# Optimization experiments

Measured on AMD Instinct MI355X. Metric: run time of the kernel, lower is better.

Reference implementation:

```python
import jax, jax.numpy as jnp
import numpy as np


def _relative_position_index(ws):
    # matches SpatialAttention.build with qWh=qWw=kWh=kWw=ws
    coords = np.stack(np.meshgrid(np.arange(ws), np.arange(ws), indexing='ij'))
    cf = coords.reshape(2, -1)  # [2, N]
    rel = (cf[:, :, None] - cf[:, None, :]).transpose(1, 2, 0)  # [N, N, 2]
    rel[:, :, 0] += ws - 1
    rel[:, :, 1] += ws - 1
    rel[:, :, 0] *= 2 * ws - 1
    return rel.sum(-1)  # [N, N] int in [0, (2*ws-1)^2)


def _shift_mask(H, W, ws, ss):
    # standard Swin shifted-window attention mask: [num_windows, N, N]
    img = np.zeros((H, W))
    cnt = 0
    for h in (slice(0, -ws), slice(-ws, -ss), slice(-ss, None)):
        for w in (slice(0, -ws), slice(-ws, -ss), slice(-ss, None)):
            img[h, w] = cnt
            cnt += 1
    win = img.reshape(H // ws, ws, W // ws, ws).transpose(0, 2, 1, 3).reshape(-1, ws * ws)
    diff = win[:, None, :] - win[:, :, None]
    return np.where(diff != 0, -100.0, 0.0).astype(np.float32)


def _window_partition(x, ws):
    B, H, W, C = x.shape
    x = x.reshape(B, H // ws, ws, W // ws, ws, C)
    x = x.transpose(0, 1, 3, 2, 4, 5)
    return x.reshape(-1, ws, ws, C)  # [B*nW, ws, ws, C]


def _window_reverse(x, ws, H, W):
    C = x.shape[-1]
    x = x.reshape(-1, H // ws, W // ws, ws, ws, C)
    x = x.transpose(0, 1, 3, 2, 4, 5)
    return x.reshape(-1, H, W, C)


def setup_inputs() -> dict:
    key = jax.random.key(0)
    k1, k2, k3, k4 = jax.random.split(key, 4)
    B, H, W, C = 16, 64, 64, 512
    num_heads, ws = 16, 8
    return {
        'q': jax.random.normal(k1, (B, H, W, C), dtype=jnp.float32),
        'k': jax.random.normal(k2, (B, H, W, C), dtype=jnp.float32),
        'v': jax.random.normal(k3, (B, H, W, C), dtype=jnp.float32),
        'bias_table': jax.random.normal(k4, ((2 * ws - 1) ** 2, num_heads), dtype=jnp.float32) * 0.02,
        'num_heads': num_heads,
        'window_size': ws,
        'shift_size': 4,
    }


def reference(q, k, v, bias_table, num_heads, window_size, shift_size):
    B, H, W, C = q.shape
    ws, ss = window_size, shift_size
    N = ws * ws
    hd = C // num_heads
    scale = hd ** -0.5

    # cyclic shift
    q = jnp.roll(q, (-ss, -ss), axis=(1, 2))
    k = jnp.roll(k, (-ss, -ss), axis=(1, 2))
    v = jnp.roll(v, (-ss, -ss), axis=(1, 2))

    # window partition -> [B*nW, heads, N, hd]
    def to_heads(x):
        x = _window_partition(x, ws).reshape(-1, N, num_heads, hd)
        return x.transpose(0, 2, 1, 3)

    qh, kh, vh = to_heads(q), to_heads(k), to_heads(v)

    attn = jnp.einsum('bhid,bhjd->bhij', qh * scale, kh)  # [BnW, h, N, N]

    # gathered relative position bias: [1, h, N, N]
    idx = jnp.asarray(_relative_position_index(ws))
    rel_bias = bias_table[idx.reshape(-1)].reshape(N, N, num_heads).transpose(2, 0, 1)
    attn = attn + rel_bias[None]

    # shifted-window mask: [nW, N, N]
    mask = jnp.asarray(_shift_mask(H, W, ws, ss))
    nW = mask.shape[0]
    attn = attn.reshape(-1, nW, num_heads, N, N) + mask[None, :, None]
    attn = attn.reshape(-1, num_heads, N, N)

    attn = jax.nn.softmax(attn, axis=-1)

    x = jnp.einsum('bhij,bhjd->bihd', attn, vh).reshape(-1, ws, ws, C)
    x = _window_reverse(x, ws, H, W)
    x = jnp.roll(x, (ss, ss), axis=(1, 2))  # reverse cyclic shift
    return x
```

## Files before the change

### kernel.cpp

```cpp
#include <hip/hip_runtime.h>

#define TB 16
#define NHEADS 16
#define HD 32
#define WS 8
#define SS 4

typedef __attribute__((ext_vector_type(8))) __bf16 bf16x8;
typedef __attribute__((ext_vector_type(4))) float f32x4;

#define OFF_Q 0
#define OFF_K 5120
#define OFF_P 0
#define OFF_V 10240
#define OFF_B 14848

__global__ void prep_bias(const float* __restrict__ bt, float* __restrict__ biasT) {
    const int t = blockIdx.x * 256 + threadIdx.x;
    const int head = t >> 12;
    const int j = (t >> 6) & 63;
    const int i = t & 63;
    const int idx = ((i >> 3) - (j >> 3) + 7) * 15 + ((i & 7) - (j & 7) + 7);
    biasT[t] = bt[idx * NHEADS + head];
}

template<bool PRE>
__global__ __launch_bounds__(256, 8)
void swin_attn_mfma(const float* __restrict__ q,
                    const float* __restrict__ k,
                    const float* __restrict__ v,
                    const float* __restrict__ bias_table,
                    const float* __restrict__ biasT,
                    float* __restrict__ out)
{
    __shared__ __align__(16) char smem[15760];
    char* sQ = smem + OFF_Q;
    char* sK = smem + OFF_K;
    char* sP = smem + OFF_P;
    char* sV = smem + OFF_V;
    float* sB = (float*)(smem + OFF_B);

    const int blk  = blockIdx.x;
    const int head = blk & (NHEADS - 1);
    const int win  = (blk >> 4) & 63;
    const int b    = blk >> 10;
    const int wh   = win >> 3;
    const int ww   = win & 7;

    const int tid  = threadIdx.x;
    const int wave = tid >> 6;
    const int lane = tid & 63;
    const int quad = lane >> 4, lm = lane & 15;

    {
        const int ih = lane >> 3, iw = lane & 7;
        const int gh = (wh * WS + ih + SS) & 63;
        const int gw = (ww * WS + iw + SS) & 63;
        const size_t rowbase = (((size_t)b * 64 + gh) * 64 + gw) * 512 + (size_t)head * HD;

        if (wave == 0) {
            const float scale = 0.17677669529663687f;
            const float4* qrow = (const float4*)(q + rowbase);
            #pragma unroll
            for (int t = 0; t < 4; ++t) {
                float4 a = qrow[2 * t], c = qrow[2 * t + 1];
                bf16x8 w;
                w[0] = (__bf16)(a.x * scale); w[1] = (__bf16)(a.y * scale);
                w[2] = (__bf16)(a.z * scale); w[3] = (__bf16)(a.w * scale);
                w[4] = (__bf16)(c.x * scale); w[5] = (__bf16)(c.y * scale);
                w[6] = (__bf16)(c.z * scale); w[7] = (__bf16)(c.w * scale);
                *(bf16x8*)(sQ + lane * 80 + 16 * t) = w;
            }
        } else if (wave == 1) {
            const float4* krow = (const float4*)(k + rowbase);
            #pragma unroll
            for (int t = 0; t < 4; ++t) {
                float4 a = krow[2 * t], c = krow[2 * t + 1];
                bf16x8 w;
                w[0] = (__bf16)a.x; w[1] = (__bf16)a.y;
                w[2] = (__bf16)a.z; w[3] = (__bf16)a.w;
                w[4] = (__bf16)c.x; w[5] = (__bf16)c.y;
                w[6] = (__bf16)c.z; w[7] = (__bf16)c.w;
                *(bf16x8*)(sK + lane * 80 + 16 * t) = w;
            }
        } else {
            const int t0 = (wave == 2) ? 0 : 4;
            const float4* vrow = (const float4*)(v + rowbase);
            #pragma unroll
            for (int t = 0; t < 4; ++t) {
                float4 x = vrow[t0 + t];
                const int ch = 4 * (t0 + t);
                *(__bf16*)(sV + (ch + 0) * 144 + lane * 2) = (__bf16)x.x;
                *(__bf16*)(sV + (ch + 1) * 144 + lane * 2) = (__bf16)x.y;
                *(__bf16*)(sV + (ch + 2) * 144 + lane * 2) = (__bf16)x.z;
                *(__bf16*)(sV + (ch + 3) * 144 + lane * 2) = (__bf16)x.w;
            }
            if (!PRE && wave == 3) {
                #pragma unroll
                for (int t = lane; t < 225; t += 64)
                    sB[t] = bias_table[t * NHEADS + head];
            }
        }
    }
    __syncthreads();

    bf16x8 qa = *(const bf16x8*)(sQ + (16 * wave + lm) * 80 + quad * 16);
    bf16x8 kb[4];
    #pragma unroll
    for (int nt = 0; nt < 4; ++nt)
        kb[nt] = *(const bf16x8*)(sK + (16 * nt + lm) * 80 + quad * 16);

    f32x4 S[4];
    #pragma unroll
    for (int nt = 0; nt < 4; ++nt) {
        f32x4 z = {0.f, 0.f, 0.f, 0.f};
        S[nt] = __builtin_amdgcn_mfma_f32_16x16x32_bf16(qa, kb[nt], z, 0, 0, 0);
    }

    const bool eh = (wh == 7), ew = (ww == 7);
    const int ihh  = 2 * wave + (quad >> 1);
    const int iww0 = 4 * (quad & 1);
    const int jw   = lm & 7;
    const float* bTh = biasT + ((size_t)head << 12);
    float part[4] = {0.f, 0.f, 0.f, 0.f};
    #pragma unroll
    for (int nt = 0; nt < 4; ++nt) {
        const int jh = 2 * nt + (lm >> 3);
        const bool okh = !eh || ((ihh < 4) == (jh < 4));
        f32x4 b4;
        if (PRE) {
            b4 = *(const f32x4*)(bTh + (16 * nt + lm) * 64 + 16 * wave + 4 * quad);
        } else {
            #pragma unroll
            for (int r = 0; r < 4; ++r)
                b4[r] = sB[(ihh - jh + 7) * 15 + (iww0 + r - jw + 7)];
        }
        #pragma unroll
        for (int r = 0; r < 4; ++r) {
            const int iww = iww0 + r;
            float s = S[nt][r] + b4[r];
            bool ok = okh && (!ew || ((iww < 4) == (jw < 4)));
            float e = ok ? __expf(s) : 0.f;
            S[nt][r] = e;
            part[r] += e;
        }
    }

    __syncthreads();
    #pragma unroll
    for (int nt = 0; nt < 4; ++nt)
        #pragma unroll
        for (int r = 0; r < 4; ++r)
            *(__bf16*)(sP + (16 * wave + 4 * quad + r) * 144 + (16 * nt + lm) * 2)
                = (__bf16)S[nt][r];
    #pragma unroll
    for (int m = 1; m <= 8; m <<= 1)
        #pragma unroll
        for (int r = 0; r < 4; ++r)
            part[r] += __shfl_xor(part[r], m, 64);
    float rl[4];
    #pragma unroll
    for (int r = 0; r < 4; ++r)
        rl[r] = 1.f / part[r];
    __syncthreads();

    bf16x8 pa0 = *(const bf16x8*)(sP + (16 * wave + lm) * 144 + quad * 16);
    bf16x8 pa1 = *(const bf16x8*)(sP + (16 * wave + lm) * 144 + 64 + quad * 16);
    bf16x8 vb[2][2];
    #pragma unroll
    for (int nt = 0; nt < 2; ++nt)
        #pragma unroll
        for (int ks = 0; ks < 2; ++ks)
            vb[nt][ks] = *(const bf16x8*)(sV + (16 * nt + lm) * 144 + ks * 64 + quad * 16);

    f32x4 O[2];
    #pragma unroll
    for (int nt = 0; nt < 2; ++nt) {
        f32x4 z = {0.f, 0.f, 0.f, 0.f};
        z = __builtin_amdgcn_mfma_f32_16x16x32_bf16(pa0, vb[nt][0], z, 0, 0, 0);
        O[nt] = __builtin_amdgcn_mfma_f32_16x16x32_bf16(pa1, vb[nt][1], z, 0, 0, 0);
    }

    #pragma unroll
    for (int r = 0; r < 4; ++r) {
        const int i = 16 * wave + 4 * quad + r;
        const int ghh = (wh * WS + (i >> 3) + SS) & 63;
        const int gww = (ww * WS + (i & 7) + SS) & 63;
        float* rp = out + (((size_t)b * 64 + ghh) * 64 + gww) * 512 + (size_t)head * HD + lm;
        rp[0]  = O[0][r] * rl[r];
        rp[16] = O[1][r] * rl[r];
    }
}

extern "C" void kernel_launch(void* const* d_in, const int* in_sizes, int n_in,
                              void* d_out, int out_size, void* d_ws, size_t ws_size,
                              hipStream_t stream) {
    const float* q  = (const float*)d_in[0];
    const float* k  = (const float*)d_in[1];
    const float* v  = (const float*)d_in[2];
    const float* bt = (const float*)d_in[3];
    float* out = (float*)d_out;
    float* biasT = (float*)d_ws;

    const bool pre = (d_ws != nullptr) && (ws_size >= (size_t)NHEADS * 64 * 64 * sizeof(float));
    dim3 block(256);
    if (pre) {
        prep_bias<<<dim3(256), block, 0, stream>>>(bt, biasT);
        swin_attn_mfma<true><<<dim3(TB * 64 * NHEADS), block, 0, stream>>>(q, k, v, bt, biasT, out);
    } else {
        swin_attn_mfma<false><<<dim3(TB * 64 * NHEADS), block, 0, stream>>>(q, k, v, bt, biasT, out);
    }
}
```

Baseline: 439.8 us.

## Process a row of eight windows per block with register-prefetched loads

Each block now handles all eight windows along one window row for a given batch and head, instead of a single window. The next window's q/k/v slice is loaded into registers while the current one is computed, and the relative-position bias is gathered once per block into registers. The separate bias-prep kernel and its launch go away. The cost is fewer blocks (2048), more registers per thread with launch bounds lowered to 5, and an extra barrier per iteration.

```diff
diff --git a/kernel.cpp b/kernel.cpp
--- a/kernel.cpp
+++ b/kernel.cpp
@@ -5,6 +5,7 @@
 #define HD 32
 #define WS 8
 #define SS 4
+#define PPB 8
 
 typedef __attribute__((ext_vector_type(8))) __bf16 bf16x8;
 typedef __attribute__((ext_vector_type(4))) float f32x4;
@@ -13,57 +14,66 @@
 #define OFF_K 5120
 #define OFF_P 0
 #define OFF_V 10240
-#define OFF_B 14848
-
-__global__ void prep_bias(const float* __restrict__ bt, float* __restrict__ biasT) {
-    const int t = blockIdx.x * 256 + threadIdx.x;
-    const int head = t >> 12;
-    const int j = (t >> 6) & 63;
-    const int i = t & 63;
-    const int idx = ((i >> 3) - (j >> 3) + 7) * 15 + ((i & 7) - (j & 7) + 7);
-    biasT[t] = bt[idx * NHEADS + head];
-}
-
-template<bool PRE>
-__global__ __launch_bounds__(256, 8)
+
+__global__ __launch_bounds__(256, 5)
 void swin_attn_mfma(const float* __restrict__ q,
                     const float* __restrict__ k,
                     const float* __restrict__ v,
                     const float* __restrict__ bias_table,
-                    const float* __restrict__ biasT,
                     float* __restrict__ out)
 {
-    __shared__ __align__(16) char smem[15760];
+    __shared__ __align__(16) char smem[14848];
     char* sQ = smem + OFF_Q;
     char* sK = smem + OFF_K;
     char* sP = smem + OFF_P;
     char* sV = smem + OFF_V;
-    float* sB = (float*)(smem + OFF_B);
-
-    const int blk  = blockIdx.x;
-    const int head = blk & (NHEADS - 1);
-    const int win  = (blk >> 4) & 63;
-    const int b    = blk >> 10;
-    const int wh   = win >> 3;
-    const int ww   = win & 7;
+
+    const int beta = blockIdx.x;
+    const int head = beta & (NHEADS - 1);
+    const int wh   = (beta >> 4) & 7;
+    const int b    = beta >> 7;
 
     const int tid  = threadIdx.x;
     const int wave = tid >> 6;
     const int lane = tid & 63;
     const int quad = lane >> 4, lm = lane & 15;
+    const int ih = lane >> 3, iw = lane & 7;
+    const int gh = (wh * WS + ih + SS) & 63;
+
+    const int ihh  = 2 * wave + (quad >> 1);
+    const int iww0 = 4 * (quad & 1);
+    const int jw   = lm & 7;
+    f32x4 bias[4];
+    #pragma unroll
+    for (int nt = 0; nt < 4; ++nt) {
+        const int jh = 2 * nt + (lm >> 3);
+        #pragma unroll
+        for (int r = 0; r < 4; ++r)
+            bias[nt][r] = bias_table[((ihh - jh + 7) * 15 + (iww0 + r - jw + 7)) * NHEADS + head];
+    }
+    const bool eh = (wh == 7);
+
+    const float* base = (wave == 0) ? q : (wave == 1) ? k : v;
+    const int t0 = (wave == 3) ? 4 : 0;
+    const size_t rowpre = ((size_t)(b * 64 + gh)) * 64;
+
+    float4 R[8];
 
     {
-        const int ih = lane >> 3, iw = lane & 7;
-        const int gh = (wh * WS + ih + SS) & 63;
-        const int gw = (ww * WS + iw + SS) & 63;
-        const size_t rowbase = (((size_t)b * 64 + gh) * 64 + gw) * 512 + (size_t)head * HD;
+        const int gw = (iw + SS) & 63;
+        const float4* src = (const float4*)(base + (rowpre + gw) * 512 + head * HD) + t0;
+        R[0] = src[0]; R[1] = src[1]; R[2] = src[2]; R[3] = src[3];
+        if (wave < 2) { R[4] = src[4]; R[5] = src[5]; R[6] = src[6]; R[7] = src[7]; }
+    }
+
+    for (int it = 0; it < PPB; ++it) {
+        __syncthreads();
 
         if (wave == 0) {
             const float scale = 0.17677669529663687f;
-            const float4* qrow = (const float4*)(q + rowbase);
             #pragma unroll
             for (int t = 0; t < 4; ++t) {
-                float4 a = qrow[2 * t], c = qrow[2 * t + 1];
+                float4 a = R[2 * t], c = R[2 * t + 1];
                 bf16x8 w;
                 w[0] = (__bf16)(a.x * scale); w[1] = (__bf16)(a.y * scale);
                 w[2] = (__bf16)(a.z * scale); w[3] = (__bf16)(a.w * scale);
@@ -72,10 +82,9 @@
                 *(bf16x8*)(sQ + lane * 80 + 16 * t) = w;
             }
         } else if (wave == 1) {
-            const float4* krow = (const float4*)(k + rowbase);
             #pragma unroll
             for (int t = 0; t < 4; ++t) {
-                float4 a = krow[2 * t], c = krow[2 * t + 1];
+                float4 a = R[2 * t], c = R[2 * t + 1];
                 bf16x8 w;
                 w[0] = (__bf16)a.x; w[1] = (__bf16)a.y;
                 w[2] = (__bf16)a.z; w[3] = (__bf16)a.w;
@@ -84,111 +93,99 @@
                 *(bf16x8*)(sK + lane * 80 + 16 * t) = w;
             }
         } else {
-            const int t0 = (wave == 2) ? 0 : 4;
-            const float4* vrow = (const float4*)(v + rowbase);
             #pragma unroll
             for (int t = 0; t < 4; ++t) {
-                float4 x = vrow[t0 + t];
+                float4 x = R[t];
                 const int ch = 4 * (t0 + t);
                 *(__bf16*)(sV + (ch + 0) * 144 + lane * 2) = (__bf16)x.x;
                 *(__bf16*)(sV + (ch + 1) * 144 + lane * 2) = (__bf16)x.y;
                 *(__bf16*)(sV + (ch + 2) * 144 + lane * 2) = (__bf16)x.z;
                 *(__bf16*)(sV + (ch + 3) * 144 + lane * 2) = (__bf16)x.w;
             }
-            if (!PRE && wave == 3) {
-                #pragma unroll
-                for (int t = lane; t < 225; t += 64)
-                    sB[t] = bias_table[t * NHEADS + head];
-            }
-        }
-    }
-    __syncthreads();
-
-    bf16x8 qa = *(const bf16x8*)(sQ + (16 * wave + lm) * 80 + quad * 16);
-    bf16x8 kb[4];
-    #pragma unroll
-    for (int nt = 0; nt < 4; ++nt)
-        kb[nt] = *(const bf16x8*)(sK + (16 * nt + lm) * 80 + quad * 16);
-
-    f32x4 S[4];
-    #pragma unroll
-    for (int nt = 0; nt < 4; ++nt) {
-        f32x4 z = {0.f, 0.f, 0.f, 0.f};
-        S[nt] = __builtin_amdgcn_mfma_f32_16x16x32_bf16(qa, kb[nt], z, 0, 0, 0);
-    }
-
-    const bool eh = (wh == 7), ew = (ww == 7);
-    const int ihh  = 2 * wave + (quad >> 1);
-    const int iww0 = 4 * (quad & 1);
-    const int jw   = lm & 7;
-    const float* bTh = biasT + ((size_t)head << 12);
-    float part[4] = {0.f, 0.f, 0.f, 0.f};
-    #pragma unroll
-    for (int nt = 0; nt < 4; ++nt) {
-        const int jh = 2 * nt + (lm >> 3);
-        const bool okh = !eh || ((ihh < 4) == (jh < 4));
-        f32x4 b4;
-        if (PRE) {
-            b4 = *(const f32x4*)(bTh + (16 * nt + lm) * 64 + 16 * wave + 4 * quad);
-        } else {
+        }
+
+        if (it + 1 < PPB) {
+            const int gw = ((it + 1) * WS + iw + SS) & 63;
+            const float4* src = (const float4*)(base + (rowpre + gw) * 512 + head * HD) + t0;
+            R[0] = src[0]; R[1] = src[1]; R[2] = src[2]; R[3] = src[3];
+            if (wave < 2) { R[4] = src[4]; R[5] = src[5]; R[6] = src[6]; R[7] = src[7]; }
+        }
+        __syncthreads();
+
+        bf16x8 qa = *(const bf16x8*)(sQ + (16 * wave + lm) * 80 + quad * 16);
+        bf16x8 kb[4];
+        #pragma unroll
+        for (int nt = 0; nt < 4; ++nt)
+            kb[nt] = *(const bf16x8*)(sK + (16 * nt + lm) * 80 + quad * 16);
+
+        f32x4 S[4];
+        #pragma unroll
+        for (int nt = 0; nt < 4; ++nt) {
+            f32x4 z = {0.f, 0.f, 0.f, 0.f};
+            S[nt] = __builtin_amdgcn_mfma_f32_16x16x32_bf16(qa, kb[nt], z, 0, 0, 0);
+        }
+
+        const bool ew = (it == PPB - 1);
+        float part[4] = {0.f, 0.f, 0.f, 0.f};
+        #pragma unroll
+        for (int nt = 0; nt < 4; ++nt) {
+            const int jh = 2 * nt + (lm >> 3);
+            const bool okh = !eh || ((ihh < 4) == (jh < 4));
+            #pragma unroll
+            for (int r = 0; r < 4; ++r) {
+                const int iww = iww0 + r;
+                float s = S[nt][r] + bias[nt][r];
+                bool ok = okh && (!ew || ((iww < 4) == (jw < 4)));
+                float e = ok ? __expf(s) : 0.f;
+                S[nt][r] = e;
+                part[r] += e;
+            }
+        }
+        __syncthreads();
+
+        #pragma unroll
+        for (int nt = 0; nt < 4; ++nt)
             #pragma unroll
             for (int r = 0; r < 4; ++r)
-                b4[r] = sB[(ihh - jh + 7) * 15 + (iww0 + r - jw + 7)];
-        }
+                *(__bf16*)(sP + (16 * wave + 4 * quad + r) * 144 + (16 * nt + lm) * 2)
+                    = (__bf16)S[nt][r];
+        #pragma unroll
+        for (int m = 1; m <= 8; m <<= 1)
+            #pragma unroll
+            for (int r = 0; r < 4; ++r)
+                part[r] += __shfl_xor(part[r], m, 64);
+        float rl[4];
+        #pragma unroll
+        for (int r = 0; r < 4; ++r)
+            rl[r] = 1.f / part[r];
+        __syncthreads();
+
+        bf16x8 pa0 = *(const bf16x8*)(sP + (16 * wave + lm) * 144 + quad * 16);
+        bf16x8 pa1 = *(const bf16x8*)(sP + (16 * wave + lm) * 144 + 64 + quad * 16);
+        bf16x8 vb[2][2];
+        #pragma unroll
+        for (int nt = 0; nt < 2; ++nt)
+            #pragma unroll
+            for (int ks = 0; ks < 2; ++ks)
+                vb[nt][ks] = *(const bf16x8*)(sV + (16 * nt + lm) * 144 + ks * 64 + quad * 16);
+
+        f32x4 O[2];
+        #pragma unroll
+        for (int nt = 0; nt < 2; ++nt) {
+            f32x4 z = {0.f, 0.f, 0.f, 0.f};
+            z = __builtin_amdgcn_mfma_f32_16x16x32_bf16(pa0, vb[nt][0], z, 0, 0, 0);
+            O[nt] = __builtin_amdgcn_mfma_f32_16x16x32_bf16(pa1, vb[nt][1], z, 0, 0, 0);
+        }
+
         #pragma unroll
         for (int r = 0; r < 4; ++r) {
-            const int iww = iww0 + r;
-            float s = S[nt][r] + b4[r];
-            bool ok = okh && (!ew || ((iww < 4) == (jw < 4)));
-            float e = ok ? __expf(s) : 0.f;
-            S[nt][r] = e;
-            part[r] += e;
-        }
-    }
-
-    __syncthreads();
-    #pragma unroll
-    for (int nt = 0; nt < 4; ++nt)
-        #pragma unroll
-        for (int r = 0; r < 4; ++r)
-            *(__bf16*)(sP + (16 * wave + 4 * quad + r) * 144 + (16 * nt + lm) * 2)
-                = (__bf16)S[nt][r];
-    #pragma unroll
-    for (int m = 1; m <= 8; m <<= 1)
-        #pragma unroll
-        for (int r = 0; r < 4; ++r)
-            part[r] += __shfl_xor(part[r], m, 64);
-    float rl[4];
-    #pragma unroll
-    for (int r = 0; r < 4; ++r)
-        rl[r] = 1.f / part[r];
-    __syncthreads();
-
-    bf16x8 pa0 = *(const bf16x8*)(sP + (16 * wave + lm) * 144 + quad * 16);
-    bf16x8 pa1 = *(const bf16x8*)(sP + (16 * wave + lm) * 144 + 64 + quad * 16);
-    bf16x8 vb[2][2];
-    #pragma unroll
-    for (int nt = 0; nt < 2; ++nt)
-        #pragma unroll
-        for (int ks = 0; ks < 2; ++ks)
-            vb[nt][ks] = *(const bf16x8*)(sV + (16 * nt + lm) * 144 + ks * 64 + quad * 16);
-
-    f32x4 O[2];
-    #pragma unroll
-    for (int nt = 0; nt < 2; ++nt) {
-        f32x4 z = {0.f, 0.f, 0.f, 0.f};
-        z = __builtin_amdgcn_mfma_f32_16x16x32_bf16(pa0, vb[nt][0], z, 0, 0, 0);
-        O[nt] = __builtin_amdgcn_mfma_f32_16x16x32_bf16(pa1, vb[nt][1], z, 0, 0, 0);
-    }
-
-    #pragma unroll
-    for (int r = 0; r < 4; ++r) {
-        const int i = 16 * wave + 4 * quad + r;
-        const int ghh = (wh * WS + (i >> 3) + SS) & 63;
-        const int gww = (ww * WS + (i & 7) + SS) & 63;
-        float* rp = out + (((size_t)b * 64 + ghh) * 64 + gww) * 512 + (size_t)head * HD + lm;
-        rp[0]  = O[0][r] * rl[r];
-        rp[16] = O[1][r] * rl[r];
+            const int i = 16 * wave + 4 * quad + r;
+            const int ghh = (wh * WS + (i >> 3) + SS) & 63;
+            const int gww = (it * WS + (i & 7) + SS) & 63;
+            float* rp = out + (((size_t)b * 64 + ghh) * 64 + gww) * 512 + (size_t)head * HD + lm;
+            rp[0]  = O[0][r] * rl[r];
+            rp[16] = O[1][r] * rl[r];
+        }
     }
 }
 
@@ -200,14 +197,8 @@
     const float* v  = (const float*)d_in[2];
     const float* bt = (const float*)d_in[3];
     float* out = (float*)d_out;
-    float* biasT = (float*)d_ws;
-
-    const bool pre = (d_ws != nullptr) && (ws_size >= (size_t)NHEADS * 64 * 64 * sizeof(float));
+
+    dim3 grid(TB * 64 * NHEADS / PPB);
     dim3 block(256);
-    if (pre) {
-        prep_bias<<<dim3(256), block, 0, stream>>>(bt, biasT);
-        swin_attn_mfma<true><<<dim3(TB * 64 * NHEADS), block, 0, stream>>>(q, k, v, bt, biasT, out);
-    } else {
-        swin_attn_mfma<false><<<dim3(TB * 64 * NHEADS), block, 0, stream>>>(q, k, v, bt, biasT, out);
-    }
+    swin_attn_mfma<<<grid, block, 0, stream>>>(q, k, v, bt, out);
 }
```

Result: no change. 441.6 us (+0.4%).
